# Performance work log

Hardware: AMD Instinct MI355X
Metric: run time of the kernel (lower is better)

## Reference

```python
import jax, jax.numpy as jnp
import numpy as np

B, S, H, NH, HD, I = 2, 1024, 4096, 32, 128, 11008
EPS = 1e-6
THETA = 10000.0


def _rmsnorm(x, w):
    v = jnp.mean(x * x, axis=-1, keepdims=True)
    return x * jax.lax.rsqrt(v + EPS) * w


def _quant(x):
    # per-tensor symmetric int8 quantization (scale already folded upstream)
    return jnp.clip(jnp.round(x), -128.0, 127.0)


def _lin_i8(xq_i8, w_i8, scale, bias):
    acc = jnp.matmul(xq_i8.astype(jnp.int32), w_i8.astype(jnp.int32).T)
    return acc.astype(jnp.float32) * scale + bias


def _rope(q, k):
    pos = jnp.arange(S, dtype=jnp.float32)
    inv = 1.0 / (THETA ** (jnp.arange(0, HD, 2, dtype=jnp.float32) / HD))
    f = pos[:, None] * inv[None, :]              # [S, HD/2]
    emb = jnp.concatenate([f, f], axis=-1)        # [S, HD]
    cos = jnp.cos(emb)[None, None]                # [1,1,S,HD]
    sin = jnp.sin(emb)[None, None]
    def rot(x):
        return jnp.concatenate([-x[..., HD // 2:], x[..., :HD // 2]], axis=-1)
    return q * cos + rot(q) * sin, k * cos + rot(k) * sin


def setup_inputs() -> dict:
    key = jax.random.key(0)
    ks = jax.random.split(key, 30)
    def w8(k, o, i):
        return jax.random.randint(k, (o, i), -128, 128, dtype=jnp.int8)
    def sc(k):
        return jax.random.uniform(k, (), jnp.float32, 0.001, 0.01)
    return {
        "hidden_states": jax.random.normal(ks[0], (B, S, H), jnp.float32),
        "ln1_w": jax.random.uniform(ks[1], (H,), jnp.float32, 0.5, 1.5) * 20.0,
        "ln2_w": jax.random.uniform(ks[2], (H,), jnp.float32, 0.5, 1.5) * 20.0,
        "Wq": w8(ks[3], H, H), "Wk": w8(ks[4], H, H), "Wv": w8(ks[5], H, H),
        "Wo": w8(ks[6], H, H),
        "Wg": w8(ks[7], I, H), "Wu": w8(ks[8], I, H), "Wd": w8(ks[9], H, I),
        "bq": jax.random.normal(ks[10], (H,), jnp.float32) * 0.01,
        "bk": jax.random.normal(ks[11], (H,), jnp.float32) * 0.01,
        "bv": jax.random.normal(ks[12], (H,), jnp.float32) * 0.01,
        "bo": jax.random.normal(ks[13], (H,), jnp.float32) * 0.01,
        "bg": jax.random.normal(ks[14], (I,), jnp.float32) * 0.01,
        "bu": jax.random.normal(ks[15], (I,), jnp.float32) * 0.01,
        "bd": jax.random.normal(ks[16], (H,), jnp.float32) * 0.01,
        "sq": sc(ks[17]) * 1e-3, "sk": sc(ks[18]) * 1e-3, "sv": sc(ks[19]) * 1e-3,
        "so": sc(ks[20]) * 1e-3, "sg": sc(ks[21]) * 1e-3, "su": sc(ks[22]) * 1e-3,
        "sd": sc(ks[23]) * 1e-3,
        "o_in_scale": sc(ks[24]), "down_in_scale": sc(ks[25]),
    }


def reference(hidden_states, ln1_w, ln2_w, Wq, Wk, Wv, Wo, Wg, Wu, Wd,
              bq, bk, bv, bo, bg, bu, bd,
              sq, sk, sv, so, sg, su, sd, o_in_scale, down_in_scale):
    residual = hidden_states
    # input RMSNorm (quant scale folded into ln1_w) -> int8 activation
    hq = _quant(_rmsnorm(hidden_states, ln1_w)).astype(jnp.int8)
    q = _lin_i8(hq, Wq, sq, bq).reshape(B, S, NH, HD).transpose(0, 2, 1, 3)
    k = _lin_i8(hq, Wk, sk, bk).reshape(B, S, NH, HD).transpose(0, 2, 1, 3)
    v = _lin_i8(hq, Wv, sv, bv).reshape(B, S, NH, HD).transpose(0, 2, 1, 3)
    q, k = _rope(q, k)
    scores = jnp.einsum("bhqd,bhkd->bhqk", q, k) / np.float32(np.sqrt(HD))
    causal = jnp.tril(jnp.ones((S, S), dtype=bool))
    scores = jnp.where(causal[None, None], scores, jnp.float32(-1e30))
    attn = jax.nn.softmax(scores, axis=-1)
    o = jnp.einsum("bhqk,bhkd->bhqd", attn, v).transpose(0, 2, 1, 3).reshape(B, S, H)
    # o_proj with quant scale (W8A8BFP32OFP32LinearWithQuantScale)
    oq = _quant(o / o_in_scale).astype(jnp.int8)
    h = residual + _lin_i8(oq, Wo, so, bo)
    residual = h
    # post-attention RMSNorm (fc1 quant scale folded into ln2_w)
    hq2 = _quant(_rmsnorm(h, ln2_w)).astype(jnp.int8)
    g = _lin_i8(hq2, Wg, sg, bg)
    u = _lin_i8(hq2, Wu, su, bu)
    a = jax.nn.silu(g) * u
    aq = _quant(a / down_in_scale).astype(jnp.int8)
    out = residual + _lin_i8(aq, Wd, sd, bd)
    return out
```

## Files before the change

kernel.cpp:

```cpp
#include <hip/hip_runtime.h>
#include <math.h>

#define B_  2
#define S_  1024
#define H_  4096
#define NH_ 32
#define HD_ 128
#define I_  11008
#define R_  2048

typedef __attribute__((ext_vector_type(4))) int i32x4;
typedef __attribute__((ext_vector_type(4))) float f32x4;
typedef __attribute__((ext_vector_type(8))) short bf16x8;


__device__ __forceinline__ void gload_lds16(const void* g, void* l) {
    __builtin_amdgcn_global_load_lds(
        (const __attribute__((address_space(1))) unsigned int*)g,
        (__attribute__((address_space(3))) unsigned int*)l, 16, 0, 0);
}

__device__ __forceinline__ unsigned short f2bf(float f) {
    unsigned int u = __float_as_uint(f);
    u += 0x7fffu + ((u >> 16) & 1u);
    return (unsigned short)(u >> 16);
}

__global__ __launch_bounds__(256)
void packW_k(const int* __restrict__ W, signed char* __restrict__ out, const int K)
{
    const int kt = blockIdx.x, cb = blockIdx.y, nk = gridDim.x;
    const int t = threadIdx.x;
    int* otile = (int*)(out + ((long)(cb * nk + kt) << 13));
#pragma unroll
    for (int i = 0; i < 8; ++i) {
        const int o = i * 256 + t;
        const int g = o >> 9, r = (o >> 2) & 127, jj = o & 3;
        const int4 w4 = *(const int4*)(W + (long)(cb * 128 + r) * K + kt * 64 + g * 16 + jj * 4);
        otile[o] = (w4.x & 255) | ((w4.y & 255) << 8) | ((w4.z & 255) << 16) | (w4.w << 24);
    }
}

__global__ __launch_bounds__(256)
void rmsnorm_quant_k(const float* __restrict__ x, const float* __restrict__ w,
                     signed char* __restrict__ out)
{
    __shared__ float red[4];
    const int tid = threadIdx.x;
    const long row = blockIdx.x;
    const float4* xr = (const float4*)(x + row * H_);
    float4 xv[4];
    float ss = 0.f;
#pragma unroll
    for (int i = 0; i < 4; ++i) {
        xv[i] = xr[tid + i * 256];
        ss += xv[i].x * xv[i].x + xv[i].y * xv[i].y
            + xv[i].z * xv[i].z + xv[i].w * xv[i].w;
    }
#pragma unroll
    for (int off = 32; off; off >>= 1) ss += __shfl_xor(ss, off);
    if ((tid & 63) == 0) red[tid >> 6] = ss;
    __syncthreads();
    const float tot = red[0] + red[1] + red[2] + red[3];
    const float sc = 1.f / sqrtf(tot * (1.f / (float)H_) + 1e-6f);
    const float4* wr = (const float4*)w;
    int* ob = (int*)out;
    const long rb = row >> 7;
    const int rr = (int)(row & 127);
#pragma unroll
    for (int i = 0; i < 4; ++i) {
        const float4 wv = wr[tid + i * 256];
        const int b0 = (int)fminf(fmaxf(rintf(xv[i].x * sc * wv.x), -128.f), 127.f);
        const int b1 = (int)fminf(fmaxf(rintf(xv[i].y * sc * wv.y), -128.f), 127.f);
        const int b2 = (int)fminf(fmaxf(rintf(xv[i].z * sc * wv.z), -128.f), 127.f);
        const int b3 = (int)fminf(fmaxf(rintf(xv[i].w * sc * wv.w), -128.f), 127.f);
        const int packed = (b0 & 255) | ((b1 & 255) << 8) | ((b2 & 255) << 16) | (b3 << 24);
        const int j4 = tid + i * 256;
        const long a32 = ((rb * 64 + (j4 >> 4)) << 11) + (((j4 >> 2) & 3) << 9)
                       + (rr << 2) + (j4 & 3);
        ob[a32] = packed;
    }
}

template<int MODE>
__global__ __launch_bounds__(256, 2)
void gemm_i8t(const signed char* __restrict__ A8, const signed char* __restrict__ W8,
              const float* __restrict__ scale_ptr, const float* __restrict__ bias,
              const float* __restrict__ residual, float* __restrict__ C,
              const float* __restrict__ gbuf, const float* __restrict__ qscale,
              signed char* __restrict__ out8,
              const int N, const int K, const int gx)
{
    __shared__ __align__(16) signed char lsA[2][16384];
    __shared__ __align__(16) signed char lsB[2][16384];

    int bid = blockIdx.x;
    {
        const int nwg = gridDim.x;
        const int q = nwg >> 3, r = nwg & 7;
        const int xcd = bid & 7, idx = bid >> 3;
        bid = (xcd < r) ? (xcd * (q + 1) + idx)
                        : (r * (q + 1) + (xcd - r) * q + idx);
    }
    const int bx = bid % gx, by = bid / gx;

    const int tid  = threadIdx.x;
    const int lane = tid & 63, wid = tid >> 6;
    const int bm = bx << 7, bn = by << 7;
    const int wm = (wid >> 1) << 6, wn = (wid & 1) << 6;

    i32x4 acc[4][4];
#pragma unroll
    for (int m = 0; m < 4; ++m)
#pragma unroll
        for (int n = 0; n < 4; ++n) acc[m][n] = (i32x4){0, 0, 0, 0};

    const int nk  = K >> 6;
    const int nk2 = K >> 7;
    const signed char* abase = A8 + ((long)bx * nk << 13);
    const signed char* bbase = W8 + ((long)by * nk << 13);
    const int sgg = wid * 4096 + lane * 16;
    const int sgl = wid * 4096;

#pragma unroll
    for (int c = 0; c < 4; ++c) {
        gload_lds16(abase + sgg + c * 1024, lsA[0] + sgl + c * 1024);
        gload_lds16(bbase + sgg + c * 1024, lsB[0] + sgl + c * 1024);
    }

    for (int kt = 0; kt < nk2; ++kt) {
        const int cur = kt & 1, nxt = cur ^ 1;
        if (kt + 1 < nk2) {
            const signed char* at = abase + ((long)(kt + 1) << 14);
            const signed char* bt = bbase + ((long)(kt + 1) << 14);
#pragma unroll
            for (int c = 0; c < 4; ++c) {
                gload_lds16(at + sgg + c * 1024, lsA[nxt] + sgl + c * 1024);
                gload_lds16(bt + sgg + c * 1024, lsB[nxt] + sgl + c * 1024);
            }
            asm volatile("s_waitcnt vmcnt(8)" ::: "memory");
        } else {
            asm volatile("s_waitcnt vmcnt(0)" ::: "memory");
        }
        __builtin_amdgcn_s_barrier();

        const int kg = (lane >> 4) * 2048, fr = (lane & 15) * 16;
#pragma unroll
        for (int s = 0; s < 2; ++s) {
            const int off = s * 8192;
            i32x4 af[4], bf[4];
#pragma unroll
            for (int m = 0; m < 4; ++m)
                af[m] = *(const i32x4*)(lsA[cur] + off + kg + wm * 16 + m * 256 + fr);
#pragma unroll
            for (int n = 0; n < 4; ++n)
                bf[n] = *(const i32x4*)(lsB[cur] + off + kg + wn * 16 + n * 256 + fr);
            __builtin_amdgcn_s_setprio(1);
#pragma unroll
            for (int m = 0; m < 4; ++m)
#pragma unroll
                for (int n = 0; n < 4; ++n)
                    acc[m][n] = __builtin_amdgcn_mfma_i32_16x16x64_i8(af[m], bf[n], acc[m][n], 0, 0, 0);
            __builtin_amdgcn_s_setprio(0);
        }
        __builtin_amdgcn_s_barrier();
    }

    const float s = *scale_ptr;
    const int rq = (lane >> 4) * 4, fc = lane & 15;
    if (MODE == 0) {
#pragma unroll
        for (int m = 0; m < 4; ++m) {
#pragma unroll
            for (int n = 0; n < 4; ++n) {
                const int col = bn + wn + n * 16 + fc;
                const float bcol = bias[col];
#pragma unroll
                for (int r = 0; r < 4; ++r) {
                    const int row = bm + wm + m * 16 + rq + r;
                    float v = (float)acc[m][n][r] * s + bcol;
                    if (residual) v += residual[(long)row * N + col];
                    C[(long)row * N + col] = v;
                }
            }
        }
    } else {
        const float dinv = 1.f / qscale[0];
        const int nko = N >> 6;
#pragma unroll
        for (int m = 0; m < 4; ++m) {
#pragma unroll
            for (int n = 0; n < 4; ++n) {
                const int col = bn + wn + n * 16 + fc;
                const float bcol = bias[col];
                const int ktc = col >> 6, kgc = (col >> 4) & 3, jc = col & 15;
#pragma unroll
                for (int r = 0; r < 4; ++r) {
                    const int row = bm + wm + m * 16 + rq + r;
                    const float u = (float)acc[m][n][r] * s + bcol;
                    const float g = gbuf[(long)row * N + col];
                    const float a = g / (1.f + __expf(-g)) * u;
                    const float qv = fminf(fmaxf(rintf(a * dinv), -128.f), 127.f);
                    const long addr = (((long)(row >> 7) * nko + ktc) << 13)
                                    + (kgc << 11) + ((row & 127) << 4) + jc;
                    out8[addr] = (signed char)(int)qv;
                }
            }
        }
    }
}

__global__ __launch_bounds__(256)
void rope_k(float* __restrict__ q, float* __restrict__ k)
{
    const int row = blockIdx.x;
    const int s = row & (S_ - 1);
    float* qr = q + (long)row * H_;
    float* kr = k + (long)row * H_;
    for (int t = threadIdx.x; t < NH_ * 64; t += 256) {
        const int nh = t >> 6, i = t & 63;
        const float inv = powf(10000.f, -(float)(2 * i) * (1.f / 128.f));
        const float f = (float)s * inv;
        float sn, c;
        sincosf(f, &sn, &c);
        const int base = nh * 128 + i;
        const float q0 = qr[base], q1 = qr[base + 64];
        qr[base]      = q0 * c - q1 * sn;
        qr[base + 64] = q1 * c + q0 * sn;
        const float k0 = kr[base], k1 = kr[base + 64];
        kr[base]      = k0 * c - k1 * sn;
        kr[base + 64] = k1 * c + k0 * sn;
    }
}

__global__ __launch_bounds__(256, 2)
void attn_mfma_k(const float* __restrict__ q, const float* __restrict__ k,
                 const float* __restrict__ v, signed char* __restrict__ out8,
                 const float* __restrict__ osc)
{
    __shared__ __align__(16) char lsK[8192];
    __shared__ __align__(16) char lsV[10240];
    __shared__ __align__(16) char lsP[4][1024];

    const int tid = threadIdx.x, lane = tid & 63, wid = tid >> 6;
    const int bid = blockIdx.x;
    const int qt = 15 - (bid >> 6);
    const int bh = bid & 63;
    const int b = bh >> 5, h = bh & 31;
    const int q0 = qt * 64;
    const int qw = q0 + wid * 16;

    const float* qbase = q + (long)(b * S_) * H_ + (long)h * HD_;
    const float* kbase = k + (long)(b * S_) * H_ + (long)h * HD_;
    const float* vbase = v + (long)(b * S_) * H_ + (long)h * HD_;

    const int frow = lane & 15, fgrp = lane >> 4;
    const float sc = 0.08838834764831845f;

    bf16x8 qf[4];
    {
        const float* qr = qbase + (long)(qw + frow) * H_;
#pragma unroll
        for (int c = 0; c < 4; ++c) {
            const float4 a = *(const float4*)(qr + c * 32 + fgrp * 8);
            const float4 bq = *(const float4*)(qr + c * 32 + fgrp * 8 + 4);
            bf16x8 t;
            t[0] = (short)f2bf(a.x * sc);  t[1] = (short)f2bf(a.y * sc);
            t[2] = (short)f2bf(a.z * sc);  t[3] = (short)f2bf(a.w * sc);
            t[4] = (short)f2bf(bq.x * sc); t[5] = (short)f2bf(bq.y * sc);
            t[6] = (short)f2bf(bq.z * sc); t[7] = (short)f2bf(bq.w * sc);
            qf[c] = t;
        }
    }

    f32x4 oacc[8];
#pragma unroll
    for (int n2 = 0; n2 < 8; ++n2) oacc[n2] = (f32x4){0.f, 0.f, 0.f, 0.f};
    float mr[4] = {-1e30f, -1e30f, -1e30f, -1e30f};
    float lr[4] = {0.f, 0.f, 0.f, 0.f};

    const int nt = (q0 >> 5) + 2;
    for (int kt = 0; kt < nt; ++kt) {
        if (kt) __syncthreads();
        {
            const float* kg = kbase + (long)(kt * 32) * H_;
            const float* vg = vbase + (long)(kt * 32) * H_;
#pragma unroll
            for (int i = 0; i < 4; ++i) {
                const int lin = i * 256 + tid;
                const int kr = lin >> 5;
                const int d4 = (lin & 31) * 4;
                const float4 kv = *(const float4*)(kg + (long)kr * H_ + d4);
                const float4 vv = *(const float4*)(vg + (long)kr * H_ + d4);
                ushort4 kb;
                kb.x = f2bf(kv.x); kb.y = f2bf(kv.y); kb.z = f2bf(kv.z); kb.w = f2bf(kv.w);
                *(ushort4*)(lsK + kr * 256 + ((d4 * 2) ^ ((kr & 7) << 4))) = kb;
                *(unsigned short*)(lsV + (d4 + 0) * 80 + kr * 2) = f2bf(vv.x);
                *(unsigned short*)(lsV + (d4 + 1) * 80 + kr * 2) = f2bf(vv.y);
                *(unsigned short*)(lsV + (d4 + 2) * 80 + kr * 2) = f2bf(vv.z);
                *(unsigned short*)(lsV + (d4 + 3) * 80 + kr * 2) = f2bf(vv.w);
            }
        }
        __syncthreads();

        if (kt * 32 <= qw + 15) {
            f32x4 s0 = (f32x4){0.f, 0.f, 0.f, 0.f};
            f32x4 s1 = (f32x4){0.f, 0.f, 0.f, 0.f};
            const int swz = (frow & 7) << 4;
#pragma unroll
            for (int c = 0; c < 4; ++c) {
                const int dby = c * 64 + fgrp * 16;
                const bf16x8 kfA = *(const bf16x8*)(lsK + frow * 256 + (dby ^ swz));
                const bf16x8 kfB = *(const bf16x8*)(lsK + (frow + 16) * 256 + (dby ^ swz));
                s0 = __builtin_amdgcn_mfma_f32_16x16x32_bf16(qf[c], kfA, s0, 0, 0, 0);
                s1 = __builtin_amdgcn_mfma_f32_16x16x32_bf16(qf[c], kfB, s1, 0, 0, 0);
            }

            const int colg0 = kt * 32 + frow;
            float cf[4];
#pragma unroll
            for (int r = 0; r < 4; ++r) {
                const int rowg = qw + fgrp * 4 + r;
                const float a0 = (colg0 <= rowg) ? s0[r] : -1e30f;
                const float a1 = (colg0 + 16 <= rowg) ? s1[r] : -1e30f;
                float mx = fmaxf(a0, a1);
#pragma unroll
                for (int off2 = 1; off2 < 16; off2 <<= 1) mx = fmaxf(mx, __shfl_xor(mx, off2));
                const float mnew = fmaxf(mr[r], mx);
                cf[r] = __expf(mr[r] - mnew);
                mr[r] = mnew;
                const float p0 = __expf(a0 - mnew);
                const float p1 = __expf(a1 - mnew);
                float sm = p0 + p1;
#pragma unroll
                for (int off2 = 1; off2 < 16; off2 <<= 1) sm += __shfl_xor(sm, off2);
                lr[r] = lr[r] * cf[r] + sm;
                const int row = fgrp * 4 + r;
                const int psw = (row & 3) << 4;
                *(unsigned short*)(lsP[wid] + row * 64 + ((frow * 2) ^ psw)) = f2bf(p0);
                *(unsigned short*)(lsP[wid] + row * 64 + (((16 + frow) * 2) ^ psw)) = f2bf(p1);
            }
#pragma unroll
            for (int n2 = 0; n2 < 8; ++n2) {
#pragma unroll
                for (int r = 0; r < 4; ++r) oacc[n2][r] *= cf[r];
            }
            const bf16x8 pf = *(const bf16x8*)(lsP[wid] + frow * 64 + ((fgrp * 16) ^ ((frow & 3) << 4)));
#pragma unroll
            for (int n2 = 0; n2 < 8; ++n2) {
                const bf16x8 vf = *(const bf16x8*)(lsV + (n2 * 16 + frow) * 80 + fgrp * 16);
                oacc[n2] = __builtin_amdgcn_mfma_f32_16x16x32_bf16(pf, vf, oacc[n2], 0, 0, 0);
            }
        }
    }

    const float oinv = 1.f / osc[0];
    float inv[4];
#pragma unroll
    for (int r = 0; r < 4; ++r) inv[r] = 1.f / lr[r];
#pragma unroll
    for (int n2 = 0; n2 < 8; ++n2) {
        const int kk = h * 128 + n2 * 16 + frow;
        const int ktc = kk >> 6, kgc = (kk >> 4) & 3, jc = kk & 15;
#pragma unroll
        for (int r = 0; r < 4; ++r) {
            const int rowt = b * S_ + qw + fgrp * 4 + r;
            const float ov = oacc[n2][r] * inv[r];
            const float qv = fminf(fmaxf(rintf(ov * oinv), -128.f), 127.f);
            const long addr = (((long)(rowt >> 7) * 64 + ktc) << 13)
                            + (kgc << 11) + ((rowt & 127) << 4) + jc;
            out8[addr] = (signed char)(int)qv;
        }
    }
}

extern "C" void kernel_launch(void* const* d_in, const int* in_sizes, int n_in,
                              void* d_out, int out_size, void* d_ws, size_t ws_size,
                              hipStream_t stream)
{
    const float* hidden = (const float*)d_in[0];
    const float* ln1 = (const float*)d_in[1];
    const float* ln2 = (const float*)d_in[2];
    const int* Wq = (const int*)d_in[3];
    const int* Wk = (const int*)d_in[4];
    const int* Wv = (const int*)d_in[5];
    const int* Wo = (const int*)d_in[6];
    const int* Wg = (const int*)d_in[7];
    const int* Wu = (const int*)d_in[8];
    const int* Wd = (const int*)d_in[9];
    const float* bq = (const float*)d_in[10];
    const float* bk = (const float*)d_in[11];
    const float* bv = (const float*)d_in[12];
    const float* bo = (const float*)d_in[13];
    const float* bg = (const float*)d_in[14];
    const float* bu = (const float*)d_in[15];
    const float* bd = (const float*)d_in[16];
    const float* sq = (const float*)d_in[17];
    const float* sk = (const float*)d_in[18];
    const float* sv = (const float*)d_in[19];
    const float* so = (const float*)d_in[20];
    const float* sg = (const float*)d_in[21];
    const float* su = (const float*)d_in[22];
    const float* sd = (const float*)d_in[23];
    const float* o_sc = (const float*)d_in[24];
    const float* d_sc = (const float*)d_in[25];

    char* ws = (char*)d_ws;
    signed char* HQ8 = (signed char*)ws;
    signed char* WP  = (signed char*)(ws + ((size_t)22 << 20));
    float* Qb = (float*)(ws + ((size_t)66 << 20));
    float* Kb = (float*)(ws + ((size_t)98 << 20));
    float* Vb = (float*)(ws + ((size_t)130 << 20));
    float* Gb = (float*)(ws + ((size_t)98 << 20));
    signed char* AQ8 = (signed char*)(ws + ((size_t)184 << 20));
    float* Hb = Qb;
    float* out = (float*)d_out;

    const dim3 blk(256);
    const int gxH = R_ / 128;
    const int nwgH = gxH * (H_ / 128);
    const int nwgI = gxH * (I_ / 128);
    const dim3 gpH(H_ / 64, H_ / 128);
    const dim3 gpI(H_ / 64, I_ / 128);
    const dim3 gpD(I_ / 64, H_ / 128);

    rmsnorm_quant_k<<<R_, blk, 0, stream>>>(hidden, ln1, HQ8);

    packW_k<<<gpH, blk, 0, stream>>>(Wq, WP, H_);
    gemm_i8t<0><<<nwgH, blk, 0, stream>>>(HQ8, WP, sq, bq, nullptr, Qb,
                                          nullptr, nullptr, nullptr, H_, H_, gxH);
    packW_k<<<gpH, blk, 0, stream>>>(Wk, WP, H_);
    gemm_i8t<0><<<nwgH, blk, 0, stream>>>(HQ8, WP, sk, bk, nullptr, Kb,
                                          nullptr, nullptr, nullptr, H_, H_, gxH);
    packW_k<<<gpH, blk, 0, stream>>>(Wv, WP, H_);
    gemm_i8t<0><<<nwgH, blk, 0, stream>>>(HQ8, WP, sv, bv, nullptr, Vb,
                                          nullptr, nullptr, nullptr, H_, H_, gxH);

    rope_k<<<R_, blk, 0, stream>>>(Qb, Kb);
    attn_mfma_k<<<B_ * NH_ * (S_ / 64), blk, 0, stream>>>(Qb, Kb, Vb, HQ8, o_sc);

    packW_k<<<gpH, blk, 0, stream>>>(Wo, WP, H_);
    gemm_i8t<0><<<nwgH, blk, 0, stream>>>(HQ8, WP, so, bo, hidden, Hb,
                                          nullptr, nullptr, nullptr, H_, H_, gxH);

    rmsnorm_quant_k<<<R_, blk, 0, stream>>>(Hb, ln2, HQ8);

    packW_k<<<gpI, blk, 0, stream>>>(Wg, WP, H_);
    gemm_i8t<0><<<nwgI, blk, 0, stream>>>(HQ8, WP, sg, bg, nullptr, Gb,
                                          nullptr, nullptr, nullptr, I_, H_, gxH);
    packW_k<<<gpI, blk, 0, stream>>>(Wu, WP, H_);
    gemm_i8t<1><<<nwgI, blk, 0, stream>>>(HQ8, WP, su, bu, nullptr, nullptr,
                                          Gb, d_sc, AQ8, I_, H_, gxH);
    packW_k<<<gpD, blk, 0, stream>>>(Wd, WP, I_);
    gemm_i8t<0><<<nwgH, blk, 0, stream>>>(AQ8, WP, sd, bd, Hb, out,
                                          nullptr, nullptr, nullptr, H_, I_, gxH);
}
```

Before: 941.4 us.

## Use 256x128 GEMM tiles with 8 waves and ping-pong phased LDS loads

```diff
diff --git a/kernel.cpp b/kernel.cpp
--- a/kernel.cpp
+++ b/kernel.cpp
@@ -31,12 +31,13 @@
 {
     const int kt = blockIdx.x, cb = blockIdx.y, nk = gridDim.x;
     const int t = threadIdx.x;
-    int* otile = (int*)(out + ((long)(cb * nk + kt) << 13));
-#pragma unroll
-    for (int i = 0; i < 8; ++i) {
+    int* otile = (int*)(out + ((long)(cb * nk + kt) << 14));
+#pragma unroll
+    for (int i = 0; i < 16; ++i) {
         const int o = i * 256 + t;
-        const int g = o >> 9, r = (o >> 2) & 127, jj = o & 3;
-        const int4 w4 = *(const int4*)(W + (long)(cb * 128 + r) * K + kt * 64 + g * 16 + jj * 4);
+        const int s = o >> 11, kg = (o >> 9) & 3, col = (o >> 2) & 127, jj = o & 3;
+        const int4 w4 = *(const int4*)(W + (long)(cb * 128 + col) * K
+                                         + kt * 128 + s * 64 + kg * 16 + jj * 4);
         otile[o] = (w4.x & 255) | ((w4.y & 255) << 8) | ((w4.z & 255) << 16) | (w4.w << 24);
     }
 }
@@ -65,7 +66,8 @@
     const float sc = 1.f / sqrtf(tot * (1.f / (float)H_) + 1e-6f);
     const float4* wr = (const float4*)w;
     int* ob = (int*)out;
-    const long rb = row >> 7;
+    const long rb = row >> 8;
+    const int hh = (int)((row >> 7) & 1);
     const int rr = (int)(row & 127);
 #pragma unroll
     for (int i = 0; i < 4; ++i) {
@@ -76,22 +78,23 @@
         const int b3 = (int)fminf(fmaxf(rintf(xv[i].w * sc * wv.w), -128.f), 127.f);
         const int packed = (b0 & 255) | ((b1 & 255) << 8) | ((b2 & 255) << 16) | (b3 << 24);
         const int j4 = tid + i * 256;
-        const long a32 = ((rb * 64 + (j4 >> 4)) << 11) + (((j4 >> 2) & 3) << 9)
-                       + (rr << 2) + (j4 & 3);
+        const int kt = j4 >> 5, sf = (j4 >> 4) & 1, kg = (j4 >> 2) & 3, jj = j4 & 3;
+        const long a32 = ((rb * 32 + kt) << 13) + (hh << 12) + (sf << 11)
+                       + (kg << 9) + (rr << 2) + jj;
         ob[a32] = packed;
     }
 }
 
 template<int MODE>
-__global__ __launch_bounds__(256, 2)
-void gemm_i8t(const signed char* __restrict__ A8, const signed char* __restrict__ W8,
+__global__ __launch_bounds__(512, 2)
+void gemm_i8p(const signed char* __restrict__ A8, const signed char* __restrict__ W8,
               const float* __restrict__ scale_ptr, const float* __restrict__ bias,
               const float* __restrict__ residual, float* __restrict__ C,
               const float* __restrict__ gbuf, const float* __restrict__ qscale,
               signed char* __restrict__ out8,
               const int N, const int K, const int gx)
 {
-    __shared__ __align__(16) signed char lsA[2][16384];
+    __shared__ __align__(16) signed char lsA[2][32768];
     __shared__ __align__(16) signed char lsB[2][16384];
 
     int bid = blockIdx.x;
@@ -103,11 +106,9 @@
                         : (r * (q + 1) + (xcd - r) * q + idx);
     }
     const int bx = bid % gx, by = bid / gx;
-
-    const int tid  = threadIdx.x;
-    const int lane = tid & 63, wid = tid >> 6;
-    const int bm = bx << 7, bn = by << 7;
-    const int wm = (wid >> 1) << 6, wn = (wid & 1) << 6;
+    const int tid = threadIdx.x, lane = tid & 63, wid = tid >> 6;
+    const int wr = wid >> 1, wc = wid & 1;
+    const int bm = bx << 8, bn = by << 7;
 
     i32x4 acc[4][4];
 #pragma unroll
@@ -115,55 +116,115 @@
 #pragma unroll
         for (int n = 0; n < 4; ++n) acc[m][n] = (i32x4){0, 0, 0, 0};
 
-    const int nk  = K >> 6;
-    const int nk2 = K >> 7;
-    const signed char* abase = A8 + ((long)bx * nk << 13);
-    const signed char* bbase = W8 + ((long)by * nk << 13);
-    const int sgg = wid * 4096 + lane * 16;
-    const int sgl = wid * 4096;
-
-#pragma unroll
-    for (int c = 0; c < 4; ++c) {
-        gload_lds16(abase + sgg + c * 1024, lsA[0] + sgl + c * 1024);
-        gload_lds16(bbase + sgg + c * 1024, lsB[0] + sgl + c * 1024);
-    }
-
-    for (int kt = 0; kt < nk2; ++kt) {
-        const int cur = kt & 1, nxt = cur ^ 1;
-        if (kt + 1 < nk2) {
-            const signed char* at = abase + ((long)(kt + 1) << 14);
-            const signed char* bt = bbase + ((long)(kt + 1) << 14);
-#pragma unroll
-            for (int c = 0; c < 4; ++c) {
-                gload_lds16(at + sgg + c * 1024, lsA[nxt] + sgl + c * 1024);
-                gload_lds16(bt + sgg + c * 1024, lsB[nxt] + sgl + c * 1024);
-            }
-            asm volatile("s_waitcnt vmcnt(8)" ::: "memory");
+    const int nk = K >> 7;
+    const signed char* abase = A8 + ((long)bx * nk << 15);
+    const signed char* bbase = W8 + ((long)by * nk << 14);
+    const int sgg = wid * 2048 + lane * 16;
+    const int sgl = wid * 2048;
+    const int la0 = (wr >> 1) * 16384 + (lane >> 4) * 2048
+                  + ((wr & 1) * 64 + (lane & 15)) * 16;
+    const int lb0 = (lane >> 4) * 2048 + (wc * 64 + (lane & 15)) * 16;
+
+    gload_lds16(abase + sgg,                lsA[0] + sgl);
+    gload_lds16(abase + sgg + 1024,         lsA[0] + sgl + 1024);
+    gload_lds16(abase + 16384 + sgg,        lsA[0] + 16384 + sgl);
+    gload_lds16(abase + 16384 + sgg + 1024, lsA[0] + 16384 + sgl + 1024);
+    gload_lds16(bbase + sgg,                lsB[0] + sgl);
+    gload_lds16(bbase + sgg + 1024,         lsB[0] + sgl + 1024);
+
+    for (int kt = 0; kt < nk; ++kt) {
+        const signed char* lA = lsA[kt & 1];
+        const signed char* lB = lsB[kt & 1];
+        signed char* nA = lsA[(kt & 1) ^ 1];
+        signed char* nB = lsB[(kt & 1) ^ 1];
+        const signed char* an = abase + ((long)(kt + 1) << 15);
+        const signed char* wn = bbase + ((long)(kt + 1) << 14);
+        const bool pf = (kt + 1 < nk);
+
+        i32x4 af0, af1, af2, af3, bf0, bf1, bf2, bf3;
+
+        if (pf) {
+            gload_lds16(an + sgg,        nA + sgl);
+            gload_lds16(an + sgg + 1024, nA + sgl + 1024);
+            asm volatile("s_waitcnt vmcnt(2)" ::: "memory");
         } else {
             asm volatile("s_waitcnt vmcnt(0)" ::: "memory");
         }
-        __builtin_amdgcn_s_barrier();
-
-        const int kg = (lane >> 4) * 2048, fr = (lane & 15) * 16;
-#pragma unroll
-        for (int s = 0; s < 2; ++s) {
-            const int off = s * 8192;
-            i32x4 af[4], bf[4];
-#pragma unroll
-            for (int m = 0; m < 4; ++m)
-                af[m] = *(const i32x4*)(lsA[cur] + off + kg + wm * 16 + m * 256 + fr);
-#pragma unroll
-            for (int n = 0; n < 4; ++n)
-                bf[n] = *(const i32x4*)(lsB[cur] + off + kg + wn * 16 + n * 256 + fr);
-            __builtin_amdgcn_s_setprio(1);
-#pragma unroll
-            for (int m = 0; m < 4; ++m)
-#pragma unroll
-                for (int n = 0; n < 4; ++n)
-                    acc[m][n] = __builtin_amdgcn_mfma_i32_16x16x64_i8(af[m], bf[n], acc[m][n], 0, 0, 0);
-            __builtin_amdgcn_s_setprio(0);
-        }
-        __builtin_amdgcn_s_barrier();
+        asm volatile("s_barrier" ::: "memory");
+        af0 = *(const i32x4*)(lA + la0);
+        af1 = *(const i32x4*)(lA + la0 + 256);
+        af2 = *(const i32x4*)(lA + la0 + 512);
+        af3 = *(const i32x4*)(lA + la0 + 768);
+        bf0 = *(const i32x4*)(lB + lb0);
+        bf1 = *(const i32x4*)(lB + lb0 + 256);
+        __builtin_amdgcn_s_setprio(1);
+        acc[0][0] = __builtin_amdgcn_mfma_i32_16x16x64_i8(af0, bf0, acc[0][0], 0, 0, 0);
+        acc[1][0] = __builtin_amdgcn_mfma_i32_16x16x64_i8(af1, bf0, acc[1][0], 0, 0, 0);
+        acc[2][0] = __builtin_amdgcn_mfma_i32_16x16x64_i8(af2, bf0, acc[2][0], 0, 0, 0);
+        acc[3][0] = __builtin_amdgcn_mfma_i32_16x16x64_i8(af3, bf0, acc[3][0], 0, 0, 0);
+        acc[0][1] = __builtin_amdgcn_mfma_i32_16x16x64_i8(af0, bf1, acc[0][1], 0, 0, 0);
+        acc[1][1] = __builtin_amdgcn_mfma_i32_16x16x64_i8(af1, bf1, acc[1][1], 0, 0, 0);
+        acc[2][1] = __builtin_amdgcn_mfma_i32_16x16x64_i8(af2, bf1, acc[2][1], 0, 0, 0);
+        acc[3][1] = __builtin_amdgcn_mfma_i32_16x16x64_i8(af3, bf1, acc[3][1], 0, 0, 0);
+        __builtin_amdgcn_s_setprio(0);
+        asm volatile("s_barrier" ::: "memory");
+
+        bf2 = *(const i32x4*)(lB + lb0 + 512);
+        bf3 = *(const i32x4*)(lB + lb0 + 768);
+        if (pf) {
+            gload_lds16(an + 16384 + sgg,        nA + 16384 + sgl);
+            gload_lds16(an + 16384 + sgg + 1024, nA + 16384 + sgl + 1024);
+        }
+        asm volatile("s_barrier" ::: "memory");
+        __builtin_amdgcn_s_setprio(1);
+        acc[0][2] = __builtin_amdgcn_mfma_i32_16x16x64_i8(af0, bf2, acc[0][2], 0, 0, 0);
+        acc[1][2] = __builtin_amdgcn_mfma_i32_16x16x64_i8(af1, bf2, acc[1][2], 0, 0, 0);
+        acc[2][2] = __builtin_amdgcn_mfma_i32_16x16x64_i8(af2, bf2, acc[2][2], 0, 0, 0);
+        acc[3][2] = __builtin_amdgcn_mfma_i32_16x16x64_i8(af3, bf2, acc[3][2], 0, 0, 0);
+        acc[0][3] = __builtin_amdgcn_mfma_i32_16x16x64_i8(af0, bf3, acc[0][3], 0, 0, 0);
+        acc[1][3] = __builtin_amdgcn_mfma_i32_16x16x64_i8(af1, bf3, acc[1][3], 0, 0, 0);
+        acc[2][3] = __builtin_amdgcn_mfma_i32_16x16x64_i8(af2, bf3, acc[2][3], 0, 0, 0);
+        acc[3][3] = __builtin_amdgcn_mfma_i32_16x16x64_i8(af3, bf3, acc[3][3], 0, 0, 0);
+        __builtin_amdgcn_s_setprio(0);
+        asm volatile("s_barrier" ::: "memory");
+
+        af0 = *(const i32x4*)(lA + la0 + 8192);
+        af1 = *(const i32x4*)(lA + la0 + 8192 + 256);
+        af2 = *(const i32x4*)(lA + la0 + 8192 + 512);
+        af3 = *(const i32x4*)(lA + la0 + 8192 + 768);
+        bf0 = *(const i32x4*)(lB + lb0 + 8192);
+        bf1 = *(const i32x4*)(lB + lb0 + 8192 + 256);
+        if (pf) {
+            gload_lds16(wn + sgg,        nB + sgl);
+            gload_lds16(wn + sgg + 1024, nB + sgl + 1024);
+        }
+        asm volatile("s_barrier" ::: "memory");
+        __builtin_amdgcn_s_setprio(1);
+        acc[0][0] = __builtin_amdgcn_mfma_i32_16x16x64_i8(af0, bf0, acc[0][0], 0, 0, 0);
+        acc[1][0] = __builtin_amdgcn_mfma_i32_16x16x64_i8(af1, bf0, acc[1][0], 0, 0, 0);
+        acc[2][0] = __builtin_amdgcn_mfma_i32_16x16x64_i8(af2, bf0, acc[2][0], 0, 0, 0);
+        acc[3][0] = __builtin_amdgcn_mfma_i32_16x16x64_i8(af3, bf0, acc[3][0], 0, 0, 0);
+        acc[0][1] = __builtin_amdgcn_mfma_i32_16x16x64_i8(af0, bf1, acc[0][1], 0, 0, 0);
+        acc[1][1] = __builtin_amdgcn_mfma_i32_16x16x64_i8(af1, bf1, acc[1][1], 0, 0, 0);
+        acc[2][1] = __builtin_amdgcn_mfma_i32_16x16x64_i8(af2, bf1, acc[2][1], 0, 0, 0);
+        acc[3][1] = __builtin_amdgcn_mfma_i32_16x16x64_i8(af3, bf1, acc[3][1], 0, 0, 0);
+        __builtin_amdgcn_s_setprio(0);
+        asm volatile("s_barrier" ::: "memory");
+
+        bf2 = *(const i32x4*)(lB + lb0 + 8192 + 512);
+        bf3 = *(const i32x4*)(lB + lb0 + 8192 + 768);
+        asm volatile("s_barrier" ::: "memory");
+        __builtin_amdgcn_s_setprio(1);
+        acc[0][2] = __builtin_amdgcn_mfma_i32_16x16x64_i8(af0, bf2, acc[0][2], 0, 0, 0);
+        acc[1][2] = __builtin_amdgcn_mfma_i32_16x16x64_i8(af1, bf2, acc[1][2], 0, 0, 0);
+        acc[2][2] = __builtin_amdgcn_mfma_i32_16x16x64_i8(af2, bf2, acc[2][2], 0, 0, 0);
+        acc[3][2] = __builtin_amdgcn_mfma_i32_16x16x64_i8(af3, bf2, acc[3][2], 0, 0, 0);
+        acc[0][3] = __builtin_amdgcn_mfma_i32_16x16x64_i8(af0, bf3, acc[0][3], 0, 0, 0);
+        acc[1][3] = __builtin_amdgcn_mfma_i32_16x16x64_i8(af1, bf3, acc[1][3], 0, 0, 0);
+        acc[2][3] = __builtin_amdgcn_mfma_i32_16x16x64_i8(af2, bf3, acc[2][3], 0, 0, 0);
+        acc[3][3] = __builtin_amdgcn_mfma_i32_16x16x64_i8(af3, bf3, acc[3][3], 0, 0, 0);
+        __builtin_amdgcn_s_setprio(0);
+        asm volatile("s_barrier" ::: "memory");
     }
 
     const float s = *scale_ptr;
@@ -173,11 +234,11 @@
         for (int m = 0; m < 4; ++m) {
 #pragma unroll
             for (int n = 0; n < 4; ++n) {
-                const int col = bn + wn + n * 16 + fc;
+                const int col = bn + wc * 64 + n * 16 + fc;
                 const float bcol = bias[col];
 #pragma unroll
                 for (int r = 0; r < 4; ++r) {
-                    const int row = bm + wm + m * 16 + rq + r;
+                    const int row = bm + wr * 64 + m * 16 + rq + r;
                     float v = (float)acc[m][n][r] * s + bcol;
                     if (residual) v += residual[(long)row * N + col];
                     C[(long)row * N + col] = v;
@@ -186,23 +247,26 @@
         }
     } else {
         const float dinv = 1.f / qscale[0];
-        const int nko = N >> 6;
+        const int nko = N >> 7;
 #pragma unroll
         for (int m = 0; m < 4; ++m) {
 #pragma unroll
             for (int n = 0; n < 4; ++n) {
-                const int col = bn + wn + n * 16 + fc;
+                const int col = bn + wc * 64 + n * 16 + fc;
                 const float bcol = bias[col];
-                const int ktc = col >> 6, kgc = (col >> 4) & 3, jc = col & 15;
+                const int kt2 = col >> 7, sf = (col >> 6) & 1;
+                const int kg2 = (col >> 4) & 3, jc = col & 15;
 #pragma unroll
                 for (int r = 0; r < 4; ++r) {
-                    const int row = bm + wm + m * 16 + rq + r;
+                    const int row = bm + wr * 64 + m * 16 + rq + r;
                     const float u = (float)acc[m][n][r] * s + bcol;
                     const float g = gbuf[(long)row * N + col];
                     const float a = g / (1.f + __expf(-g)) * u;
                     const float qv = fminf(fmaxf(rintf(a * dinv), -128.f), 127.f);
-                    const long addr = (((long)(row >> 7) * nko + ktc) << 13)
-                                    + (kgc << 11) + ((row & 127) << 4) + jc;
+                    const long addr = (((long)(row >> 8) * nko + kt2) << 15)
+                                    + ((long)((row >> 7) & 1) << 14)
+                                    + (sf << 13) + (kg2 << 11)
+                                    + ((row & 127) << 4) + jc;
                     out8[addr] = (signed char)(int)qv;
                 }
             }
@@ -361,14 +425,15 @@
 #pragma unroll
     for (int n2 = 0; n2 < 8; ++n2) {
         const int kk = h * 128 + n2 * 16 + frow;
-        const int ktc = kk >> 6, kgc = (kk >> 4) & 3, jc = kk & 15;
+        const int kt2 = kk >> 7, sf = (kk >> 6) & 1, kg = (kk >> 4) & 3, jc = kk & 15;
 #pragma unroll
         for (int r = 0; r < 4; ++r) {
             const int rowt = b * S_ + qw + fgrp * 4 + r;
             const float ov = oacc[n2][r] * inv[r];
             const float qv = fminf(fmaxf(rintf(ov * oinv), -128.f), 127.f);
-            const long addr = (((long)(rowt >> 7) * 64 + ktc) << 13)
-                            + (kgc << 11) + ((rowt & 127) << 4) + jc;
+            const long addr = (((long)(rowt >> 8) * 32 + kt2) << 15)
+                            + ((long)((rowt >> 7) & 1) << 14)
+                            + (sf << 13) + (kg << 11) + ((rowt & 127) << 4) + jc;
             out8[addr] = (signed char)(int)qv;
         }
     }
@@ -417,41 +482,42 @@
     float* out = (float*)d_out;
 
     const dim3 blk(256);
-    const int gxH = R_ / 128;
-    const int nwgH = gxH * (H_ / 128);
-    const int nwgI = gxH * (I_ / 128);
-    const dim3 gpH(H_ / 64, H_ / 128);
-    const dim3 gpI(H_ / 64, I_ / 128);
-    const dim3 gpD(I_ / 64, H_ / 128);
+    const dim3 blk5(512);
+    const int gxM = R_ / 256;
+    const int nwgH = gxM * (H_ / 128);
+    const int nwgI = gxM * (I_ / 128);
+    const dim3 gpH(H_ / 128, H_ / 128);
+    const dim3 gpI(H_ / 128, I_ / 128);
+    const dim3 gpD(I_ / 128, H_ / 128);
 
     rmsnorm_quant_k<<<R_, blk, 0, stream>>>(hidden, ln1, HQ8);
 
     packW_k<<<gpH, blk, 0, stream>>>(Wq, WP, H_);
-    gemm_i8t<0><<<nwgH, blk, 0, stream>>>(HQ8, WP, sq, bq, nullptr, Qb,
-                                          nullptr, nullptr, nullptr, H_, H_, gxH);
+    gemm_i8p<0><<<nwgH, blk5, 0, stream>>>(HQ8, WP, sq, bq, nullptr, Qb,
+                                           nullptr, nullptr, nullptr, H_, H_, gxM);
     packW_k<<<gpH, blk, 0, stream>>>(Wk, WP, H_);
-    gemm_i8t<0><<<nwgH, blk, 0, stream>>>(HQ8, WP, sk, bk, nullptr, Kb,
-                                          nullptr, nullptr, nullptr, H_, H_, gxH);
+    gemm_i8p<0><<<nwgH, blk5, 0, stream>>>(HQ8, WP, sk, bk, nullptr, Kb,
+                                           nullptr, nullptr, nullptr, H_, H_, gxM);
     packW_k<<<gpH, blk, 0, stream>>>(Wv, WP, H_);
-    gemm_i8t<0><<<nwgH, blk, 0, stream>>>(HQ8, WP, sv, bv, nullptr, Vb,
-                                          nullptr, nullptr, nullptr, H_, H_, gxH);
+    gemm_i8p<0><<<nwgH, blk5, 0, stream>>>(HQ8, WP, sv, bv, nullptr, Vb,
+                                           nullptr, nullptr, nullptr, H_, H_, gxM);
 
     rope_k<<<R_, blk, 0, stream>>>(Qb, Kb);
     attn_mfma_k<<<B_ * NH_ * (S_ / 64), blk, 0, stream>>>(Qb, Kb, Vb, HQ8, o_sc);
 
     packW_k<<<gpH, blk, 0, stream>>>(Wo, WP, H_);
-    gemm_i8t<0><<<nwgH, blk, 0, stream>>>(HQ8, WP, so, bo, hidden, Hb,
-                                          nullptr, nullptr, nullptr, H_, H_, gxH);
+    gemm_i8p<0><<<nwgH, blk5, 0, stream>>>(HQ8, WP, so, bo, hidden, Hb,
+                                           nullptr, nullptr, nullptr, H_, H_, gxM);
 
     rmsnorm_quant_k<<<R_, blk, 0, stream>>>(Hb, ln2, HQ8);
 
     packW_k<<<gpI, blk, 0, stream>>>(Wg, WP, H_);
-    gemm_i8t<0><<<nwgI, blk, 0, stream>>>(HQ8, WP, sg, bg, nullptr, Gb,
-                                          nullptr, nullptr, nullptr, I_, H_, gxH);
+    gemm_i8p<0><<<nwgI, blk5, 0, stream>>>(HQ8, WP, sg, bg, nullptr, Gb,
+                                           nullptr, nullptr, nullptr, I_, H_, gxM);
     packW_k<<<gpI, blk, 0, stream>>>(Wu, WP, H_);
-    gemm_i8t<1><<<nwgI, blk, 0, stream>>>(HQ8, WP, su, bu, nullptr, nullptr,
-                                          Gb, d_sc, AQ8, I_, H_, gxH);
+    gemm_i8p<1><<<nwgI, blk5, 0, stream>>>(HQ8, WP, su, bu, nullptr, nullptr,
+                                           Gb, d_sc, AQ8, I_, H_, gxM);
     packW_k<<<gpD, blk, 0, stream>>>(Wd, WP, I_);
-    gemm_i8t<0><<<nwgH, blk, 0, stream>>>(AQ8, WP, sd, bd, Hb, out,
-                                          nullptr, nullptr, nullptr, H_, I_, gxH);
-}
+    gemm_i8p<0><<<nwgH, blk5, 0, stream>>>(AQ8, WP, sd, bd, Hb, out,
+                                           nullptr, nullptr, nullptr, H_, I_, gxM);
+}
```

After: 1.152 ms. +22.4%, slower.

## Add 128x256-tile int8 GEMM for gate/up projections and raise attention occupancy

Applied to the files above, without the earlier changes.

```diff
diff --git a/kernel.cpp b/kernel.cpp
--- a/kernel.cpp
+++ b/kernel.cpp
@@ -168,19 +168,122 @@
 
     const float s = *scale_ptr;
     const int rq = (lane >> 4) * 4, fc = lane & 15;
+#pragma unroll
+    for (int m = 0; m < 4; ++m) {
+#pragma unroll
+        for (int n = 0; n < 4; ++n) {
+            const int col = bn + wn + n * 16 + fc;
+            const float bcol = bias[col];
+#pragma unroll
+            for (int r = 0; r < 4; ++r) {
+                const int row = bm + wm + m * 16 + rq + r;
+                float v = (float)acc[m][n][r] * s + bcol;
+                if (residual) v += residual[(long)row * N + col];
+                C[(long)row * N + col] = v;
+            }
+        }
+    }
+}
+
+template<int MODE>
+__global__ __launch_bounds__(256, 2)
+void gemm_i8w(const signed char* __restrict__ A8, const signed char* __restrict__ W8,
+              const float* __restrict__ scale_ptr, const float* __restrict__ bias,
+              float* __restrict__ C,
+              const float* __restrict__ gbuf, const float* __restrict__ qscale,
+              signed char* __restrict__ out8,
+              const int N, const int K, const int gx)
+{
+    __shared__ __align__(16) signed char lsA[2][8192];
+    __shared__ __align__(16) signed char lsB[2][16384];
+
+    int bid = blockIdx.x;
+    {
+        const int nwg = gridDim.x;
+        const int q = nwg >> 3, r = nwg & 7;
+        const int xcd = bid & 7, idx = bid >> 3;
+        bid = (xcd < r) ? (xcd * (q + 1) + idx)
+                        : (r * (q + 1) + (xcd - r) * q + idx);
+    }
+    const int bx = bid % gx, by = bid / gx;
+    const int tid = threadIdx.x, lane = tid & 63, wid = tid >> 6;
+    const int bm = bx << 7, bn = by << 8;
+    const int wm = (wid >> 1) << 6;
+    const int wn = (wid & 1) << 7;
+
+    i32x4 acc[4][8];
+#pragma unroll
+    for (int m = 0; m < 4; ++m)
+#pragma unroll
+        for (int n = 0; n < 8; ++n) acc[m][n] = (i32x4){0, 0, 0, 0};
+
+    const int nk = K >> 6;
+    const signed char* abase = A8 + ((long)bx * nk << 13);
+    const signed char* bbase = W8 + ((long)(2 * by) * nk << 13);
+    const int sa = wid * 2048;
+    const int sb = wid * 4096;
+
+    {
+        gload_lds16(abase + sa + lane * 16,        lsA[0] + sa);
+        gload_lds16(abase + sa + lane * 16 + 1024, lsA[0] + sa + 1024);
+#pragma unroll
+        for (int c = 0; c < 4; ++c) {
+            const int o = sb + c * 1024;
+            const long gsrc = ((long)((o >> 13) * nk) << 13) + (o & 8191);
+            gload_lds16(bbase + gsrc + lane * 16, lsB[0] + o);
+        }
+    }
+
+    for (int kt = 0; kt < nk; ++kt) {
+        const int cur = kt & 1, nxt = cur ^ 1;
+        if (kt + 1 < nk) {
+            const signed char* at = abase + ((long)(kt + 1) << 13);
+            gload_lds16(at + sa + lane * 16,        lsA[nxt] + sa);
+            gload_lds16(at + sa + lane * 16 + 1024, lsA[nxt] + sa + 1024);
+#pragma unroll
+            for (int c = 0; c < 4; ++c) {
+                const int o = sb + c * 1024;
+                const long gsrc = ((long)((o >> 13) * nk + (kt + 1)) << 13) + (o & 8191);
+                gload_lds16(bbase + gsrc + lane * 16, lsB[nxt] + o);
+            }
+            asm volatile("s_waitcnt vmcnt(6)" ::: "memory");
+        } else {
+            asm volatile("s_waitcnt vmcnt(0)" ::: "memory");
+        }
+        __builtin_amdgcn_s_barrier();
+
+        const int kg = (lane >> 4) * 2048, fr = (lane & 15) * 16;
+        const int bofs = (wid & 1) * 8192;
+        i32x4 af[4], bf[8];
+#pragma unroll
+        for (int m = 0; m < 4; ++m)
+            af[m] = *(const i32x4*)(lsA[cur] + kg + wm * 16 + m * 256 + fr);
+#pragma unroll
+        for (int n = 0; n < 8; ++n)
+            bf[n] = *(const i32x4*)(lsB[cur] + bofs + kg + n * 256 + fr);
+        __builtin_amdgcn_s_setprio(1);
+#pragma unroll
+        for (int m = 0; m < 4; ++m)
+#pragma unroll
+            for (int n = 0; n < 8; ++n)
+                acc[m][n] = __builtin_amdgcn_mfma_i32_16x16x64_i8(af[m], bf[n], acc[m][n], 0, 0, 0);
+        __builtin_amdgcn_s_setprio(0);
+        __builtin_amdgcn_s_barrier();
+    }
+
+    const float s = *scale_ptr;
+    const int rq = (lane >> 4) * 4, fc = lane & 15;
     if (MODE == 0) {
 #pragma unroll
         for (int m = 0; m < 4; ++m) {
 #pragma unroll
-            for (int n = 0; n < 4; ++n) {
+            for (int n = 0; n < 8; ++n) {
                 const int col = bn + wn + n * 16 + fc;
                 const float bcol = bias[col];
 #pragma unroll
                 for (int r = 0; r < 4; ++r) {
                     const int row = bm + wm + m * 16 + rq + r;
-                    float v = (float)acc[m][n][r] * s + bcol;
-                    if (residual) v += residual[(long)row * N + col];
-                    C[(long)row * N + col] = v;
+                    C[(long)row * N + col] = (float)acc[m][n][r] * s + bcol;
                 }
             }
         }
@@ -190,7 +293,7 @@
 #pragma unroll
         for (int m = 0; m < 4; ++m) {
 #pragma unroll
-            for (int n = 0; n < 4; ++n) {
+            for (int n = 0; n < 8; ++n) {
                 const int col = bn + wn + n * 16 + fc;
                 const float bcol = bias[col];
                 const int ktc = col >> 6, kgc = (col >> 4) & 3, jc = col & 15;
@@ -233,7 +336,7 @@
     }
 }
 
-__global__ __launch_bounds__(256, 2)
+__global__ __launch_bounds__(256, 3)
 void attn_mfma_k(const float* __restrict__ q, const float* __restrict__ k,
                  const float* __restrict__ v, signed char* __restrict__ out8,
                  const float* __restrict__ osc)
@@ -419,7 +522,7 @@
     const dim3 blk(256);
     const int gxH = R_ / 128;
     const int nwgH = gxH * (H_ / 128);
-    const int nwgI = gxH * (I_ / 128);
+    const int nwgW = gxH * (I_ / 256);
     const dim3 gpH(H_ / 64, H_ / 128);
     const dim3 gpI(H_ / 64, I_ / 128);
     const dim3 gpD(I_ / 64, H_ / 128);
@@ -446,10 +549,10 @@
     rmsnorm_quant_k<<<R_, blk, 0, stream>>>(Hb, ln2, HQ8);
 
     packW_k<<<gpI, blk, 0, stream>>>(Wg, WP, H_);
-    gemm_i8t<0><<<nwgI, blk, 0, stream>>>(HQ8, WP, sg, bg, nullptr, Gb,
+    gemm_i8w<0><<<nwgW, blk, 0, stream>>>(HQ8, WP, sg, bg, Gb,
                                           nullptr, nullptr, nullptr, I_, H_, gxH);
     packW_k<<<gpI, blk, 0, stream>>>(Wu, WP, H_);
-    gemm_i8t<1><<<nwgI, blk, 0, stream>>>(HQ8, WP, su, bu, nullptr, nullptr,
+    gemm_i8w<1><<<nwgW, blk, 0, stream>>>(HQ8, WP, su, bu, nullptr,
                                           Gb, d_sc, AQ8, I_, H_, gxH);
     packW_k<<<gpD, blk, 0, stream>>>(Wd, WP, I_);
     gemm_i8t<0><<<nwgH, blk, 0, stream>>>(AQ8, WP, sd, bd, Hb, out,
```

Result: no change. 959.0 us (+1.9%).

## Fuse gate and up GEMMs into one dual-accumulator kernel with SiLU epilogue

Applied to the files above, without the earlier changes.

```diff
diff --git a/kernel.cpp b/kernel.cpp
--- a/kernel.cpp
+++ b/kernel.cpp
@@ -87,8 +87,6 @@
 void gemm_i8t(const signed char* __restrict__ A8, const signed char* __restrict__ W8,
               const float* __restrict__ scale_ptr, const float* __restrict__ bias,
               const float* __restrict__ residual, float* __restrict__ C,
-              const float* __restrict__ gbuf, const float* __restrict__ qscale,
-              signed char* __restrict__ out8,
               const int N, const int K, const int gx)
 {
     __shared__ __align__(16) signed char lsA[2][16384];
@@ -168,43 +166,132 @@
 
     const float s = *scale_ptr;
     const int rq = (lane >> 4) * 4, fc = lane & 15;
-    if (MODE == 0) {
-#pragma unroll
-        for (int m = 0; m < 4; ++m) {
+#pragma unroll
+    for (int m = 0; m < 4; ++m) {
+#pragma unroll
+        for (int n = 0; n < 4; ++n) {
+            const int col = bn + wn + n * 16 + fc;
+            const float bcol = bias[col];
+#pragma unroll
+            for (int r = 0; r < 4; ++r) {
+                const int row = bm + wm + m * 16 + rq + r;
+                float v = (float)acc[m][n][r] * s + bcol;
+                if (residual) v += residual[(long)row * N + col];
+                C[(long)row * N + col] = v;
+            }
+        }
+    }
+}
+
+__global__ __launch_bounds__(256, 2)
+void gemm_gu(const signed char* __restrict__ A8, const signed char* __restrict__ G8,
+             const signed char* __restrict__ U8,
+             const float* __restrict__ sg_p, const float* __restrict__ bg,
+             const float* __restrict__ su_p, const float* __restrict__ bu,
+             const float* __restrict__ qscale, signed char* __restrict__ out8,
+             const int N, const int K, const int gx)
+{
+    __shared__ __align__(16) signed char lsA[2][8192];
+    __shared__ __align__(16) signed char lsG[2][8192];
+    __shared__ __align__(16) signed char lsU[2][8192];
+
+    int bid = blockIdx.x;
+    {
+        const int nwg = gridDim.x;
+        const int q = nwg >> 3, r = nwg & 7;
+        const int xcd = bid & 7, idx = bid >> 3;
+        bid = (xcd < r) ? (xcd * (q + 1) + idx)
+                        : (r * (q + 1) + (xcd - r) * q + idx);
+    }
+    const int bx = bid % gx, by = bid / gx;
+    const int tid = threadIdx.x, lane = tid & 63, wid = tid >> 6;
+    const int bm = bx << 7, bn = by << 7;
+    const int wm = (wid >> 1) << 6, wn = (wid & 1) << 6;
+
+    i32x4 ag[4][4], au[4][4];
+#pragma unroll
+    for (int m = 0; m < 4; ++m)
+#pragma unroll
+        for (int n = 0; n < 4; ++n) {
+            ag[m][n] = (i32x4){0, 0, 0, 0};
+            au[m][n] = (i32x4){0, 0, 0, 0};
+        }
+
+    const int nk = K >> 6;
+    const signed char* abase = A8 + ((long)bx * nk << 13);
+    const signed char* gbase = G8 + ((long)by * nk << 13);
+    const signed char* ubase = U8 + ((long)by * nk << 13);
+    const int sgg = wid * 2048 + lane * 16;
+    const int sgl = wid * 2048;
+
+#pragma unroll
+    for (int c = 0; c < 2; ++c) {
+        gload_lds16(abase + sgg + c * 1024, lsA[0] + sgl + c * 1024);
+        gload_lds16(gbase + sgg + c * 1024, lsG[0] + sgl + c * 1024);
+        gload_lds16(ubase + sgg + c * 1024, lsU[0] + sgl + c * 1024);
+    }
+
+    for (int kt = 0; kt < nk; ++kt) {
+        const int cur = kt & 1, nxt = cur ^ 1;
+        if (kt + 1 < nk) {
+            const signed char* at = abase + ((long)(kt + 1) << 13);
+            const signed char* gt = gbase + ((long)(kt + 1) << 13);
+            const signed char* ut = ubase + ((long)(kt + 1) << 13);
+#pragma unroll
+            for (int c = 0; c < 2; ++c) {
+                gload_lds16(at + sgg + c * 1024, lsA[nxt] + sgl + c * 1024);
+                gload_lds16(gt + sgg + c * 1024, lsG[nxt] + sgl + c * 1024);
+                gload_lds16(ut + sgg + c * 1024, lsU[nxt] + sgl + c * 1024);
+            }
+            asm volatile("s_waitcnt vmcnt(6)" ::: "memory");
+        } else {
+            asm volatile("s_waitcnt vmcnt(0)" ::: "memory");
+        }
+        __builtin_amdgcn_s_barrier();
+
+        const int kg = (lane >> 4) * 2048, fr = (lane & 15) * 16;
+        i32x4 af[4], gf[4], uf[4];
+#pragma unroll
+        for (int m = 0; m < 4; ++m)
+            af[m] = *(const i32x4*)(lsA[cur] + kg + wm * 16 + m * 256 + fr);
+#pragma unroll
+        for (int n = 0; n < 4; ++n) {
+            gf[n] = *(const i32x4*)(lsG[cur] + kg + wn * 16 + n * 256 + fr);
+            uf[n] = *(const i32x4*)(lsU[cur] + kg + wn * 16 + n * 256 + fr);
+        }
+        __builtin_amdgcn_s_setprio(1);
+#pragma unroll
+        for (int m = 0; m < 4; ++m)
 #pragma unroll
             for (int n = 0; n < 4; ++n) {
-                const int col = bn + wn + n * 16 + fc;
-                const float bcol = bias[col];
-#pragma unroll
-                for (int r = 0; r < 4; ++r) {
-                    const int row = bm + wm + m * 16 + rq + r;
-                    float v = (float)acc[m][n][r] * s + bcol;
-                    if (residual) v += residual[(long)row * N + col];
-                    C[(long)row * N + col] = v;
-                }
-            }
-        }
-    } else {
-        const float dinv = 1.f / qscale[0];
-        const int nko = N >> 6;
-#pragma unroll
-        for (int m = 0; m < 4; ++m) {
-#pragma unroll
-            for (int n = 0; n < 4; ++n) {
-                const int col = bn + wn + n * 16 + fc;
-                const float bcol = bias[col];
-                const int ktc = col >> 6, kgc = (col >> 4) & 3, jc = col & 15;
-#pragma unroll
-                for (int r = 0; r < 4; ++r) {
-                    const int row = bm + wm + m * 16 + rq + r;
-                    const float u = (float)acc[m][n][r] * s + bcol;
-                    const float g = gbuf[(long)row * N + col];
-                    const float a = g / (1.f + __expf(-g)) * u;
-                    const float qv = fminf(fmaxf(rintf(a * dinv), -128.f), 127.f);
-                    const long addr = (((long)(row >> 7) * nko + ktc) << 13)
-                                    + (kgc << 11) + ((row & 127) << 4) + jc;
-                    out8[addr] = (signed char)(int)qv;
-                }
+                ag[m][n] = __builtin_amdgcn_mfma_i32_16x16x64_i8(af[m], gf[n], ag[m][n], 0, 0, 0);
+                au[m][n] = __builtin_amdgcn_mfma_i32_16x16x64_i8(af[m], uf[n], au[m][n], 0, 0, 0);
+            }
+        __builtin_amdgcn_s_setprio(0);
+        __builtin_amdgcn_s_barrier();
+    }
+
+    const float sg = *sg_p, su = *su_p;
+    const float dinv = 1.f / qscale[0];
+    const int nko = N >> 6;
+    const int rq = (lane >> 4) * 4, fc = lane & 15;
+#pragma unroll
+    for (int m = 0; m < 4; ++m) {
+#pragma unroll
+        for (int n = 0; n < 4; ++n) {
+            const int col = bn + wn + n * 16 + fc;
+            const float bgc = bg[col], buc = bu[col];
+            const int ktc = col >> 6, kgc = (col >> 4) & 3, jc = col & 15;
+#pragma unroll
+            for (int r = 0; r < 4; ++r) {
+                const int row = bm + wm + m * 16 + rq + r;
+                const float g = (float)ag[m][n][r] * sg + bgc;
+                const float u = (float)au[m][n][r] * su + buc;
+                const float a = g / (1.f + __expf(-g)) * u;
+                const float qv = fminf(fmaxf(rintf(a * dinv), -128.f), 127.f);
+                const long addr = (((long)(row >> 7) * nko + ktc) << 13)
+                                + (kgc << 11) + ((row & 127) << 4) + jc;
+                out8[addr] = (signed char)(int)qv;
             }
         }
     }
@@ -233,7 +320,7 @@
     }
 }
 
-__global__ __launch_bounds__(256, 2)
+__global__ __launch_bounds__(256, 3)
 void attn_mfma_k(const float* __restrict__ q, const float* __restrict__ k,
                  const float* __restrict__ v, signed char* __restrict__ out8,
                  const float* __restrict__ osc)
@@ -411,7 +498,7 @@
     float* Qb = (float*)(ws + ((size_t)66 << 20));
     float* Kb = (float*)(ws + ((size_t)98 << 20));
     float* Vb = (float*)(ws + ((size_t)130 << 20));
-    float* Gb = (float*)(ws + ((size_t)98 << 20));
+    signed char* WPu = (signed char*)(ws + ((size_t)98 << 20));
     signed char* AQ8 = (signed char*)(ws + ((size_t)184 << 20));
     float* Hb = Qb;
     float* out = (float*)d_out;
@@ -427,31 +514,24 @@
     rmsnorm_quant_k<<<R_, blk, 0, stream>>>(hidden, ln1, HQ8);
 
     packW_k<<<gpH, blk, 0, stream>>>(Wq, WP, H_);
-    gemm_i8t<0><<<nwgH, blk, 0, stream>>>(HQ8, WP, sq, bq, nullptr, Qb,
-                                          nullptr, nullptr, nullptr, H_, H_, gxH);
+    gemm_i8t<0><<<nwgH, blk, 0, stream>>>(HQ8, WP, sq, bq, nullptr, Qb, H_, H_, gxH);
     packW_k<<<gpH, blk, 0, stream>>>(Wk, WP, H_);
-    gemm_i8t<0><<<nwgH, blk, 0, stream>>>(HQ8, WP, sk, bk, nullptr, Kb,
-                                          nullptr, nullptr, nullptr, H_, H_, gxH);
+    gemm_i8t<0><<<nwgH, blk, 0, stream>>>(HQ8, WP, sk, bk, nullptr, Kb, H_, H_, gxH);
     packW_k<<<gpH, blk, 0, stream>>>(Wv, WP, H_);
-    gemm_i8t<0><<<nwgH, blk, 0, stream>>>(HQ8, WP, sv, bv, nullptr, Vb,
-                                          nullptr, nullptr, nullptr, H_, H_, gxH);
+    gemm_i8t<0><<<nwgH, blk, 0, stream>>>(HQ8, WP, sv, bv, nullptr, Vb, H_, H_, gxH);
 
     rope_k<<<R_, blk, 0, stream>>>(Qb, Kb);
     attn_mfma_k<<<B_ * NH_ * (S_ / 64), blk, 0, stream>>>(Qb, Kb, Vb, HQ8, o_sc);
 
     packW_k<<<gpH, blk, 0, stream>>>(Wo, WP, H_);
-    gemm_i8t<0><<<nwgH, blk, 0, stream>>>(HQ8, WP, so, bo, hidden, Hb,
-                                          nullptr, nullptr, nullptr, H_, H_, gxH);
+    gemm_i8t<0><<<nwgH, blk, 0, stream>>>(HQ8, WP, so, bo, hidden, Hb, H_, H_, gxH);
 
     rmsnorm_quant_k<<<R_, blk, 0, stream>>>(Hb, ln2, HQ8);
 
     packW_k<<<gpI, blk, 0, stream>>>(Wg, WP, H_);
-    gemm_i8t<0><<<nwgI, blk, 0, stream>>>(HQ8, WP, sg, bg, nullptr, Gb,
-                                          nullptr, nullptr, nullptr, I_, H_, gxH);
-    packW_k<<<gpI, blk, 0, stream>>>(Wu, WP, H_);
-    gemm_i8t<1><<<nwgI, blk, 0, stream>>>(HQ8, WP, su, bu, nullptr, nullptr,
-                                          Gb, d_sc, AQ8, I_, H_, gxH);
+    packW_k<<<gpI, blk, 0, stream>>>(Wu, WPu, H_);
+    gemm_gu<<<nwgI, blk, 0, stream>>>(HQ8, WP, WPu, sg, bg, su, bu,
+                                      d_sc, AQ8, I_, H_, gxH);
     packW_k<<<gpD, blk, 0, stream>>>(Wd, WP, I_);
-    gemm_i8t<0><<<nwgH, blk, 0, stream>>>(AQ8, WP, sd, bd, Hb, out,
-                                          nullptr, nullptr, nullptr, H_, I_, gxH);
-}
+    gemm_i8t<0><<<nwgH, blk, 0, stream>>>(AQ8, WP, sd, bd, Hb, out, H_, I_, gxH);
+}
```

Result: no change. 932.3 us (-1.0%).
